# Kernel tuning notes

Hardware: AMD Instinct MI355X
Metric: run time of the kernel (lower is better)

Reference implementation:

```python
import jax, jax.numpy as jnp
import numpy as np

L, H, DH = 4, 8, 64            # num_layers, num_heads, hidden_dim (= dim_per_head)
HD = H * DH                    # 512 = per-layer q/k/v width
R, BLOCK, NREG, NW = 3, 128, 8, 8   # n_hashes, block_size, num_regions, num_w_per_dist
CDIM, LAT = 2, 3               # coords_dim, latent_dim
SCALE = 1.0 / float(np.sqrt(DH))


def layer_norm(x, g, b):
    m = x.mean(-1, keepdims=True)
    v = ((x - m) ** 2).mean(-1, keepdims=True)
    return (x - m) * jax.lax.rsqrt(v + 1e-5) * g + b


def hept_attention(q, k, v, coords, batch, w_head, hash_proj):
    # HEPT: E2LSH hash + region/batch bucketing -> sort -> blockwise attention
    # with RPE distance bias, combined over hash rounds by logsumexp weights.
    N = q.shape[0]
    nb = N // BLOCK
    qh = q.reshape(N, H, DH)
    kh = k.reshape(N, H, DH)
    vh = v.reshape(N, H, DH)
    c0 = coords[:, 0]
    region = jnp.clip(((c0 - c0.min()) / (c0.max() - c0.min() + 1e-6) * NREG).astype(jnp.int32), 0, NREG - 1)
    c_rpe = coords[:, 1:]                       # [N, CDIM-1] dims used for RPE distances
    bf = batch.astype(jnp.float32)
    outs, lses = [], []
    for r in range(R):
        hv = coords @ hash_proj[r]              # [N] LSH projection
        hn = (hv - hv.min()) / (hv.max() - hv.min() + 1e-6)
        skey = (bf * NREG + region.astype(jnp.float32)) * 2.0 + hn  # batch-major, region, hash
        idx = jnp.argsort(skey)
        inv = jnp.argsort(idx)
        qs = qh[idx].reshape(nb, BLOCK, H, DH)
        ks = kh[idx].reshape(nb, BLOCK, H, DH)
        vs = vh[idx].reshape(nb, BLOCK, H, DH)
        cs = c_rpe[idx].reshape(nb, BLOCK, CDIM - 1)
        bs = batch[idx].reshape(nb, BLOCK)
        scores = jnp.einsum('bihd,bjhd->bhij', qs, ks) * SCALE     # [nb,H,B,B]
        d2 = (cs[:, :, None, :] - cs[:, None, :, :]) ** 2          # [nb,B,B,CDIM-1]
        scores = scores - jnp.einsum('hc,bijc->bhij', w_head, d2)  # RPE distance penalty
        scores = jnp.where((bs[:, :, None] == bs[:, None, :])[:, None], scores, -1e9)
        lse = jax.nn.logsumexp(scores, axis=-1)                    # [nb,H,B]
        p = jnp.exp(scores - lse[..., None])
        o = jnp.einsum('bhij,bjhd->bihd', p, vs).reshape(N, H, DH)
        outs.append(o[inv])
        lses.append(jnp.transpose(lse, (0, 2, 1)).reshape(N, H)[inv])
    wts = jax.nn.softmax(jnp.stack(lses), axis=0)[..., None]       # [R,N,H,1]
    return (wts * jnp.stack(outs)).sum(0).reshape(N, HD)


def _forward(x, coords, batch, enc_W1, enc_b1, enc_W2, enc_b2, ln1_g, ln1_b, wq, wk, wv,
             rpe_W, wo, ln2_g, ln2_b, ff_W1, ff_b1, ff_W2, ff_b2, W_cat,
             mlp_W1, mlp_b1, mlp_W2, mlp_b2, beta_W1, beta_b1, beta_W2, beta_b2,
             coord_W1, coord_b1, coord_W2, coord_b2, hash_proj):
    h0 = jax.nn.relu(x @ enc_W1 + enc_b1) @ enc_W2 + enc_b2
    feats = [h0]
    cur = h0
    for l in range(L):
        xn = layer_norm(cur, ln1_g[l], ln1_b[l])
        q = xn @ wq[l]
        k = xn @ wk[l]
        v = xn @ wv[l]
        # per-head positive RPE weights derived from w_rpe weight matrix
        w_head = jax.nn.softplus(rpe_W[l].reshape(CDIM - 1, NW, H, DH).mean(axis=(1, 3)).T)  # [H,CDIM-1]
        a = hept_attention(q, k, v, coords, batch, w_head, hash_proj) @ wo[l]
        cur = cur + a
        ffo = jax.nn.relu(layer_norm(cur, ln2_g[l], ln2_b[l]) @ ff_W1[l] + ff_b1[l]) @ ff_W2[l] + ff_b2[l]
        cur = cur + ffo
        feats.append(cur)
    enc2 = jnp.concatenate(feats, axis=-1) @ W_cat
    out = enc2 + (jax.nn.relu(enc2 @ mlp_W1 + mlp_b1) @ mlp_W2 + mlp_b2)
    eps = 1e-6
    beta = jnp.clip(jax.nn.sigmoid(jax.nn.relu(out @ beta_W1 + beta_b1) @ beta_W2 + beta_b2), eps, 1.0 - eps)
    hcoord = jax.nn.relu(out @ coord_W1 + coord_b1) @ coord_W2 + coord_b2
    return beta, hcoord


def setup_inputs() -> dict:
    key = jax.random.key(0)
    ks = jax.random.split(key, 40)
    N, IN_DIM = 32768, 16
    def w(i, shape, s=0.05):
        return jax.random.normal(ks[i], shape, jnp.float32) * s
    return dict(
        x=jax.random.normal(ks[0], (N, IN_DIM), jnp.float32),
        coords=jax.random.normal(ks[1], (N, CDIM), jnp.float32),
        batch=jnp.sort(jax.random.randint(ks[2], (N,), 0, 8)),
        enc_W1=w(3, (IN_DIM, DH)), enc_b1=jnp.zeros((DH,), jnp.float32),
        enc_W2=w(4, (DH, DH)), enc_b2=jnp.zeros((DH,), jnp.float32),
        ln1_g=jnp.ones((L, DH), jnp.float32), ln1_b=jnp.zeros((L, DH), jnp.float32),
        wq=w(5, (L, DH, HD)), wk=w(6, (L, DH, HD)), wv=w(7, (L, DH, HD)),
        rpe_W=w(8, (L, NW * (CDIM - 1), HD)),
        wo=w(9, (L, HD, DH)),
        ln2_g=jnp.ones((L, DH), jnp.float32), ln2_b=jnp.zeros((L, DH), jnp.float32),
        ff_W1=w(10, (L, DH, DH)), ff_b1=jnp.zeros((L, DH), jnp.float32),
        ff_W2=w(11, (L, DH, DH)), ff_b2=jnp.zeros((L, DH), jnp.float32),
        W_cat=w(12, (DH * (L + 1), DH // 2)),
        mlp_W1=w(13, (DH // 2, DH // 2)), mlp_b1=jnp.zeros((DH // 2,), jnp.float32),
        mlp_W2=w(14, (DH // 2, DH // 2)), mlp_b2=jnp.zeros((DH // 2,), jnp.float32),
        beta_W1=w(15, (DH // 2, DH // 4)), beta_b1=jnp.zeros((DH // 4,), jnp.float32),
        beta_W2=w(16, (DH // 4, 1)), beta_b2=jnp.zeros((1,), jnp.float32),
        coord_W1=w(17, (DH // 2, DH // 4)), coord_b1=jnp.zeros((DH // 4,), jnp.float32),
        coord_W2=w(18, (DH // 4, LAT)), coord_b2=jnp.zeros((LAT,), jnp.float32),
        hash_proj=jax.random.normal(ks[19], (R, CDIM), jnp.float32),
    )


def reference(x, coords, batch, enc_W1, enc_b1, enc_W2, enc_b2, ln1_g, ln1_b, wq, wk, wv,
              rpe_W, wo, ln2_g, ln2_b, ff_W1, ff_b1, ff_W2, ff_b2, W_cat,
              mlp_W1, mlp_b1, mlp_W2, mlp_b2, beta_W1, beta_b1, beta_W2, beta_b2,
              coord_W1, coord_b1, coord_W2, coord_b2, hash_proj):
    return _forward(x, coords, batch, enc_W1, enc_b1, enc_W2, enc_b2, ln1_g, ln1_b, wq, wk, wv,
                    rpe_W, wo, ln2_g, ln2_b, ff_W1, ff_b1, ff_W2, ff_b2, W_cat,
                    mlp_W1, mlp_b1, mlp_W2, mlp_b2, beta_W1, beta_b1, beta_W2, beta_b2,
                    coord_W1, coord_b1, coord_W2, coord_b2, hash_proj)
```

## Files before the change

### kernel.cpp

```cpp
#include <hip/hip_runtime.h>
#include <math.h>

#define DEV __device__ __forceinline__

constexpr int DHc = 64;
constexpr int HDc = 512;
constexpr int Hc  = 8;
constexpr int BLKc = 128;

typedef float f32x16 __attribute__((ext_vector_type(16)));
typedef short s16x8  __attribute__((ext_vector_type(8)));

union FragU { unsigned u[4]; s16x8 v; };

DEV unsigned fenc(float f){ unsigned u = __float_as_uint(f); return (u & 0x80000000u) ? ~u : (u | 0x80000000u); }
DEV float fdec(unsigned u){ unsigned b = (u & 0x80000000u) ? (u ^ 0x80000000u) : ~u; return __uint_as_float(b); }
DEV float hv_calc(float c0, float c1, float h0, float h1){
  return __fadd_rn(__fmul_rn(c0, h0), __fmul_rn(c1, h1));
}
DEV unsigned short f2bf(float f){
  unsigned u = __float_as_uint(f);
  return (unsigned short)((u + 0x7FFFu + ((u >> 16) & 1u)) >> 16);
}
DEV float bf2f(unsigned short s){ return __uint_as_float((unsigned)s << 16); }

DEV unsigned cvtpk(float lo, float hi){
  unsigned r;
  asm("v_cvt_pk_bf16_f32 %0, %1, %2" : "=v"(r) : "v"(lo), "v"(hi));
  return r;
}
DEV void pswap(unsigned &a, unsigned &b){
  asm volatile("v_permlane32_swap_b32 %0, %1" : "+v"(a), "+v"(b));
}

__global__ void minmax_init_kernel(unsigned* mm){
  int t = threadIdx.x;
  if (t < 4) mm[t] = 0xFFFFFFFFu;
  else if (t < 8) mm[t] = 0u;
}

__global__ __launch_bounds__(256) void minmax_reduce_kernel(const float* __restrict__ coords,
    const float* __restrict__ hp, unsigned* mm, int N)
{
  __shared__ float red[4][8];
  float h[6];
  #pragma unroll
  for (int i = 0; i < 6; ++i) h[i] = hp[i];
  float mn[4] = {3.0e38f, 3.0e38f, 3.0e38f, 3.0e38f};
  float mx[4] = {-3.0e38f, -3.0e38f, -3.0e38f, -3.0e38f};
  for (int i = blockIdx.x*blockDim.x + threadIdx.x; i < N; i += gridDim.x*blockDim.x){
    float2 c = *(const float2*)&coords[2*i];
    float v0 = c.x;
    float v1 = hv_calc(c.x, c.y, h[0], h[1]);
    float v2 = hv_calc(c.x, c.y, h[2], h[3]);
    float v3 = hv_calc(c.x, c.y, h[4], h[5]);
    mn[0] = fminf(mn[0], v0); mx[0] = fmaxf(mx[0], v0);
    mn[1] = fminf(mn[1], v1); mx[1] = fmaxf(mx[1], v1);
    mn[2] = fminf(mn[2], v2); mx[2] = fmaxf(mx[2], v2);
    mn[3] = fminf(mn[3], v3); mx[3] = fmaxf(mx[3], v3);
  }
  #pragma unroll
  for (int o = 1; o < 64; o <<= 1){
    #pragma unroll
    for (int s = 0; s < 4; ++s){
      mn[s] = fminf(mn[s], __shfl_xor(mn[s], o));
      mx[s] = fmaxf(mx[s], __shfl_xor(mx[s], o));
    }
  }
  int w = threadIdx.x >> 6;
  if ((threadIdx.x & 63) == 0){
    #pragma unroll
    for (int s = 0; s < 4; ++s){ red[w][s] = mn[s]; red[w][4+s] = mx[s]; }
  }
  __syncthreads();
  int t = threadIdx.x;
  if (t < 4){
    float v = fminf(fminf(red[0][t], red[1][t]), fminf(red[2][t], red[3][t]));
    atomicMin(&mm[t], fenc(v));
  } else if (t < 8){
    float v = fmaxf(fmaxf(red[0][t], red[1][t]), fmaxf(red[2][t], red[3][t]));
    atomicMax(&mm[t], fenc(v));
  }
}

__global__ void make_keys_kernel(const float* __restrict__ coords, const int* __restrict__ batch,
                                 const float* __restrict__ hp, const unsigned* __restrict__ mm,
                                 unsigned long long* __restrict__ keys, int N)
{
  int i = blockIdx.x*blockDim.x + threadIdx.x;
  if (i >= N) return;
  float c0 = coords[2*i], c1 = coords[2*i+1];
  float c0min = fdec(mm[0]), c0max = fdec(mm[4]);
  float rf = (c0 - c0min) / (c0max - c0min + 1e-6f) * 8.0f;
  int region = (int)rf;
  region = region < 0 ? 0 : (region > 7 ? 7 : region);
  float base2 = ((float)batch[i] * 8.0f + (float)region) * 2.0f;
  #pragma unroll
  for (int r = 0; r < 3; ++r){
    float hv = hv_calc(c0, c1, hp[2*r], hp[2*r+1]);
    float hn = (hv - fdec(mm[1+r])) / (fdec(mm[5+r]) - fdec(mm[1+r]) + 1e-6f);
    float skey = base2 + hn;
    keys[(size_t)r*N + i] = ((unsigned long long)__float_as_uint(skey) << 32) | (unsigned)i;
  }
}

__global__ __launch_bounds__(1024) void bitonic_local_full2k_kernel(unsigned long long* keys, int N)
{
  __shared__ unsigned long long sh[2048];
  unsigned long long* a = keys + (size_t)blockIdx.y * N;
  int base = blockIdx.x * 2048, t = threadIdx.x;
  sh[t] = a[base + t];
  sh[t + 1024] = a[base + t + 1024];
  __syncthreads();
  for (int k = 2; k <= 2048; k <<= 1){
    for (int j = k >> 1; j > 0; j >>= 1){
      int i = ((t & ~(j-1)) << 1) | (t & (j-1));
      bool dirup = (((base + i) & k) == 0);
      unsigned long long x = sh[i], y = sh[i+j];
      if ((x > y) == dirup){ sh[i] = y; sh[i+j] = x; }
      __syncthreads();
    }
  }
  a[base + t] = sh[t];
  a[base + t + 1024] = sh[t + 1024];
}

__global__ void bitonic_global_kernel(unsigned long long* keys, int N, int k, int j)
{
  unsigned long long* a = keys + (size_t)blockIdx.y * N;
  int i = blockIdx.x*blockDim.x + threadIdx.x;
  int l = i ^ j;
  if (l > i && l < N){
    unsigned long long x = a[i], y = a[l];
    bool dirup = ((i & k) == 0);
    if ((x > y) == dirup){ a[i] = y; a[l] = x; }
  }
}

__global__ __launch_bounds__(1024) void bitonic_local_merge2k_kernel(unsigned long long* keys, int N, int k)
{
  __shared__ unsigned long long sh[2048];
  unsigned long long* a = keys + (size_t)blockIdx.y * N;
  int base = blockIdx.x * 2048, t = threadIdx.x;
  sh[t] = a[base + t];
  sh[t + 1024] = a[base + t + 1024];
  __syncthreads();
  for (int j = 1024; j > 0; j >>= 1){
    int i = ((t & ~(j-1)) << 1) | (t & (j-1));
    bool dirup = (((base + i) & k) == 0);
    unsigned long long x = sh[i], y = sh[i+j];
    if ((x > y) == dirup){ sh[i] = y; sh[i+j] = x; }
    __syncthreads();
  }
  a[base + t] = sh[t];
  a[base + t + 1024] = sh[t + 1024];
}

__global__ void extract_idx_kernel(const unsigned long long* __restrict__ keys, int* __restrict__ idx, int total)
{
  int i = blockIdx.x*blockDim.x + threadIdx.x;
  if (i < total) idx[i] = (int)(keys[i] & 0xFFFFFFFFull);
}

__global__ void wconv_kernel(const float* __restrict__ wq, const float* __restrict__ wk,
                             const float* __restrict__ wv, const float* __restrict__ wo,
                             unsigned short* __restrict__ wqkvT, unsigned short* __restrict__ woT)
{
  int tid = blockIdx.x*blockDim.x + threadIdx.x;
  const int NQ = 4*3*512*64;
  if (tid < NQ){
    int kk = tid & 63;
    int rest = tid >> 6;
    int n = rest & 511;
    int rest2 = rest >> 9;
    int z = rest2 % 3, l = rest2 / 3;
    const float* W = (z==0) ? wq : (z==1) ? wk : wv;
    wqkvT[tid] = f2bf(W[((size_t)l*64 + kk)*512 + n]);
  } else if (tid < NQ + 4*64*512){
    int e = tid - NQ;
    int kk = e & 511;
    int rest = e >> 9;
    int n = rest & 63;
    int l = rest >> 6;
    woT[e] = f2bf(wo[((size_t)l*512 + kk)*64 + n]);
  }
}

__global__ __launch_bounds__(256) void encoder_kernel(const float* __restrict__ x,
    const float* __restrict__ W1, const float* __restrict__ b1,
    const float* __restrict__ W2, const float* __restrict__ b2,
    const float* __restrict__ lng, const float* __restrict__ lnb,
    float* __restrict__ h0, unsigned short* __restrict__ xnb, int N)
{
  __shared__ float W1s[16][64];
  __shared__ __align__(16) float W2s[64][64];
  __shared__ float xs[4][16];
  __shared__ float t1s[4][64];
  int t = threadIdx.x;
  for (int f = t; f < 1024; f += 256) W1s[f>>6][f&63] = W1[f];
  #pragma unroll
  for (int e = 0; e < 4; ++e){ int f = t + e*256; *(float4*)&W2s[f>>4][(f&15)*4] = *(const float4*)&W2[f*4]; }
  int w = t >> 6, d = t & 63;
  int row = blockIdx.x*4 + w;
  if (d < 16) xs[w][d] = x[(size_t)row*16 + d];
  __syncthreads();
  float acc = b1[d];
  #pragma unroll
  for (int i = 0; i < 16; ++i) acc += xs[w][i]*W1s[i][d];
  t1s[w][d] = fmaxf(acc, 0.f);
  __syncthreads();
  float acc2 = b2[d];
  #pragma unroll
  for (int i = 0; i < 64; ++i) acc2 += t1s[w][i]*W2s[i][d];
  h0[(size_t)row*64 + d] = acc2;
  float s = acc2;
  #pragma unroll
  for (int o = 1; o < 64; o <<= 1) s += __shfl_xor(s, o);
  float mean = s * (1.0f/64.0f);
  float dv = acc2 - mean, sq = dv*dv;
  #pragma unroll
  for (int o = 1; o < 64; o <<= 1) sq += __shfl_xor(sq, o);
  xnb[(size_t)row*64 + d] = f2bf(dv * rsqrtf(sq*(1.0f/64.0f) + 1e-5f) * lng[d] + lnb[d]);
}

__global__ __launch_bounds__(256) void qkv_mfma_kernel(
    const unsigned short* __restrict__ xnb, const unsigned short* __restrict__ wqkvT_l,
    unsigned short* __restrict__ q, unsigned short* __restrict__ k, unsigned short* __restrict__ v, int N)
{
  __shared__ __align__(16) unsigned short a_lds[128*64];
  __shared__ __align__(16) unsigned short b_lds[128*64];
  int z = blockIdx.z;
  unsigned short* C = (z==0) ? q : (z==1) ? k : v;
  const unsigned short* wT = wqkvT_l + (size_t)z*512*64;
  float oscale = (z==0) ? 0.125f : 1.0f;
  int rb = blockIdx.x*128, cb = blockIdx.y*128;
  int t = threadIdx.x;
  #pragma unroll
  for (int e = 0; e < 4; ++e){
    int f = t + e*256; int row = f >> 3, ch = f & 7;
    *(s16x8*)&a_lds[row*64 + ((ch ^ (row&7))*8)] = *(const s16x8*)&xnb[(size_t)(rb+row)*64 + ch*8];
    *(s16x8*)&b_lds[row*64 + ((ch ^ (row&7))*8)] = *(const s16x8*)&wT[(size_t)(cb+row)*64 + ch*8];
  }
  __syncthreads();
  int w = t >> 6, l = t & 63, lo = l & 31, hi = l >> 5;
  s16x8 bf[4];
  #pragma unroll
  for (int ks = 0; ks < 4; ++ks){
    int brow = w*32 + lo, s = (ks<<1)|hi;
    bf[ks] = *(const s16x8*)&b_lds[brow*64 + ((s ^ (brow&7))*8)];
  }
  f32x16 acc[4];
  #pragma unroll
  for (int mt = 0; mt < 4; ++mt)
    #pragma unroll
    for (int i = 0; i < 16; ++i) acc[mt][i] = 0.f;
  #pragma unroll
  for (int mt = 0; mt < 4; ++mt){
    int arow = mt*32 + lo;
    #pragma unroll
    for (int ks = 0; ks < 4; ++ks){
      int s = (ks<<1)|hi;
      s16x8 af = *(const s16x8*)&a_lds[arow*64 + ((s ^ (arow&7))*8)];
      acc[mt] = __builtin_amdgcn_mfma_f32_32x32x16_bf16(af, bf[ks], acc[mt], 0, 0, 0);
    }
  }
  #pragma unroll
  for (int mt = 0; mt < 4; ++mt)
    #pragma unroll
    for (int reg = 0; reg < 16; ++reg){
      int m = mt*32 + (reg&3) + 8*(reg>>2) + 4*hi;
      C[(size_t)(rb+m)*HDc + cb + w*32 + lo] = f2bf(acc[mt][reg]*oscale);
    }
}

__global__ void whead_kernel(const float* __restrict__ rpe, float* __restrict__ wh)
{
  int l = blockIdx.x >> 3, h = blockIdx.x & 7, d = threadIdx.x;
  const float* rp = rpe + (size_t)l*8*512;
  float s = 0.f;
  #pragma unroll
  for (int w = 0; w < 8; ++w) s += rp[(size_t)w*512 + h*64 + d];
  #pragma unroll
  for (int o = 1; o < 64; o <<= 1) s += __shfl_xor(s, o);
  if (d == 0){
    float m = s * (1.0f/512.0f);
    wh[blockIdx.x] = fmaxf(m, 0.f) + log1pf(expf(-fabsf(m)));
  }
}

__global__ __launch_bounds__(256, 3) void attn_kernel(
    const unsigned short* __restrict__ qm, const unsigned short* __restrict__ km,
    const unsigned short* __restrict__ vm,
    const float* __restrict__ coords, const int* __restrict__ batch,
    const int* __restrict__ idx_all, const float* __restrict__ w_head,
    float* __restrict__ lse_all, unsigned short* __restrict__ o_buf, int N)
{
  __shared__ __align__(16) unsigned short qlds[128*64];
  __shared__ __align__(16) unsigned short klds[128*64];
  __shared__ __align__(16) unsigned short vtl[64*128];
  __shared__ __align__(16) float c1s[BLKc];
  __shared__ __align__(16) int   bts[BLKc];
  __shared__ int   idxs[BLKc];
  __shared__ __align__(16) float isel[BLKc];
  __shared__ int unif;
  int b = blockIdx.x, h = blockIdx.y, r = blockIdx.z, t = threadIdx.x;
  const int* idx_r = idx_all + (size_t)r*N;
  if (t < BLKc){
    int g = idx_r[b*BLKc + t];
    idxs[t] = g; c1s[t] = coords[2*g+1]; bts[t] = batch[g];
  }
  __syncthreads();
  if (t == 0) unif = (bts[0] == bts[127]);
  #pragma unroll
  for (int e = 0; e < 4; ++e){
    int f = t + e*256;
    int row = f >> 3, ch = f & 7;
    int g = idxs[row];
    s16x8 qv = *(const s16x8*)&qm[(size_t)g*HDc + h*DHc + ch*8];
    s16x8 kv = *(const s16x8*)&km[(size_t)g*HDc + h*DHc + ch*8];
    *(s16x8*)&qlds[row*64 + ((ch ^ (row&7))*8)] = qv;
    *(s16x8*)&klds[row*64 + ((ch ^ (row&7))*8)] = kv;
  }
  #pragma unroll
  for (int e = 0; e < 2; ++e){
    int pf = t + e*256;
    int jp = pf >> 3, dc = pf & 7;
    int j0 = jp*2, j1 = j0+1;
    s16x8 v0 = *(const s16x8*)&vm[(size_t)idxs[j0]*HDc + h*DHc + dc*8];
    s16x8 v1 = *(const s16x8*)&vm[(size_t)idxs[j1]*HDc + h*DHc + dc*8];
    int cj = jp >> 2;
    int jo = jp & 3;
    #pragma unroll
    for (int i = 0; i < 8; ++i){
      int d = dc*8 + i;
      unsigned val = (unsigned)(unsigned short)v0[i] | ((unsigned)(unsigned short)v1[i] << 16);
      *(unsigned*)&vtl[d*128 + ((cj ^ (d&7))*8) + jo*2] = val;
    }
  }
  __syncthreads();

  int w = t >> 6, l = t & 63, lo = l & 31, hi = l >> 5;
  int qrow = w*32 + lo;

  s16x8 qf[4];
  #pragma unroll
  for (int ks = 0; ks < 4; ++ks)
    qf[ks] = *(const s16x8*)&qlds[qrow*64 + ((((ks<<1)|hi) ^ (qrow&7))*8)];

  f32x16 acc[4];
  #pragma unroll
  for (int kt = 0; kt < 4; ++kt)
    #pragma unroll
    for (int i = 0; i < 16; ++i) acc[kt][i] = 0.f;

  __builtin_amdgcn_s_setprio(1);
  #pragma unroll
  for (int kt = 0; kt < 4; ++kt){
    int krow = kt*32 + lo;
    #pragma unroll
    for (int ks = 0; ks < 4; ++ks){
      s16x8 kf = *(const s16x8*)&klds[krow*64 + ((((ks<<1)|hi) ^ (krow&7))*8)];
      acc[kt] = __builtin_amdgcn_mfma_f32_32x32x16_bf16(kf, qf[ks], acc[kt], 0, 0, 0);
    }
  }
  __builtin_amdgcn_s_setprio(0);

  float c1i = c1s[qrow]; int bti = bts[qrow];
  float wh = w_head[h];
  int msk = unif;
  #pragma unroll
  for (int kt = 0; kt < 4; ++kt){
    #pragma unroll
    for (int rq = 0; rq < 4; ++rq){
      int kb = kt*32 + rq*8 + hi*4;
      float4 c4 = *(const float4*)&c1s[kb];
      int4  b4 = *(const int4*)&bts[kb];
      #pragma unroll
      for (int j = 0; j < 4; ++j){
        int reg = rq*4 + j;
        float c1k = (j==0)?c4.x:(j==1)?c4.y:(j==2)?c4.z:c4.w;
        int   btk = (j==0)?b4.x:(j==1)?b4.y:(j==2)?b4.z:b4.w;
        float dd = c1i - c1k;
        float sc = acc[kt][reg] - wh*dd*dd;
        if (!msk && bti != btk) sc = -1e9f;
        acc[kt][reg] = sc;
      }
    }
  }

  float m = -3.0e38f;
  #pragma unroll
  for (int kt = 0; kt < 4; ++kt)
    #pragma unroll
    for (int i = 0; i < 16; ++i) m = fmaxf(m, acc[kt][i]);
  m = fmaxf(m, __shfl_xor(m, 32));
  float se = 0.f;
  #pragma unroll
  for (int kt = 0; kt < 4; ++kt)
    #pragma unroll
    for (int i = 0; i < 16; ++i){
      float p = __expf(acc[kt][i] - m);
      acc[kt][i] = p;
      se += p;
    }
  se += __shfl_xor(se, 32);
  if (l < 32){
    int gi0 = idxs[qrow];
    lse_all[((size_t)r*N + gi0)*Hc + h] = m + __logf(se);
    isel[qrow] = 1.0f / se;
  }

  f32x16 oa0, oa1;
  #pragma unroll
  for (int i = 0; i < 16; ++i){ oa0[i] = 0.f; oa1[i] = 0.f; }

  __builtin_amdgcn_s_setprio(1);
  #pragma unroll
  for (int kt = 0; kt < 4; ++kt){
    unsigned X = cvtpk(acc[kt][0],  acc[kt][1]);
    unsigned Z = cvtpk(acc[kt][2],  acc[kt][3]);
    unsigned Y = cvtpk(acc[kt][4],  acc[kt][5]);
    unsigned W = cvtpk(acc[kt][6],  acc[kt][7]);
    pswap(X, Y); pswap(Z, W);
    FragU f0; f0.u[0]=X; f0.u[1]=Z; f0.u[2]=Y; f0.u[3]=W;
    unsigned X2 = cvtpk(acc[kt][8],  acc[kt][9]);
    unsigned Z2 = cvtpk(acc[kt][10], acc[kt][11]);
    unsigned Y2 = cvtpk(acc[kt][12], acc[kt][13]);
    unsigned W2 = cvtpk(acc[kt][14], acc[kt][15]);
    pswap(X2, Y2); pswap(Z2, W2);
    FragU f1; f1.u[0]=X2; f1.u[1]=Z2; f1.u[2]=Y2; f1.u[3]=W2;
    #pragma unroll
    for (int hks = 0; hks < 2; ++hks){
      s16x8 pa = hks ? f1.v : f0.v;
      int kch = kt*4 + hks*2 + hi;
      int d0 = lo;
      s16x8 vf0 = *(const s16x8*)&vtl[d0*128 + ((kch ^ (d0&7))*8)];
      oa0 = __builtin_amdgcn_mfma_f32_32x32x16_bf16(pa, vf0, oa0, 0, 0, 0);
      int d1 = 32 + lo;
      s16x8 vf1 = *(const s16x8*)&vtl[d1*128 + ((kch ^ (d1&7))*8)];
      oa1 = __builtin_amdgcn_mfma_f32_32x32x16_bf16(pa, vf1, oa1, 0, 0, 0);
    }
  }
  __builtin_amdgcn_s_setprio(0);

  unsigned short* orow = o_buf + (size_t)r*N*HDc;
  #pragma unroll
  for (int rq = 0; rq < 4; ++rq){
    float4 s4 = *(const float4*)&isel[w*32 + rq*8 + hi*4];
    #pragma unroll
    for (int j = 0; j < 4; ++j){
      int reg = rq*4 + j;
      int qq = rq*8 + hi*4 + j;
      int g = idxs[w*32 + qq];
      float sv = (j==0)?s4.x:(j==1)?s4.y:(j==2)?s4.z:s4.w;
      unsigned short* dst = &orow[(size_t)g*HDc + h*DHc + lo];
      dst[0]  = f2bf(oa0[reg]*sv);
      dst[32] = f2bf(oa1[reg]*sv);
    }
  }
}

__global__ __launch_bounds__(256) void wo_mfma_kernel(
    const unsigned short* __restrict__ o_buf, const float* __restrict__ lse_all,
    const unsigned short* __restrict__ woT_l, float* __restrict__ cur, int N)
{
  __shared__ __align__(16) unsigned short As[64*128];
  __shared__ __align__(16) unsigned short Bs[64*128];
  __shared__ float wts[64][24];
  int rb = blockIdx.x*64, t = threadIdx.x;
  #pragma unroll
  for (int e = 0; e < 2; ++e){
    int p = t + e*256;
    int rr = p >> 3, h = p & 7;
    float l0 = lse_all[((size_t)0*N + rb+rr)*Hc + h];
    float l1 = lse_all[((size_t)1*N + rb+rr)*Hc + h];
    float l2 = lse_all[((size_t)2*N + rb+rr)*Hc + h];
    float lm = fmaxf(l0, fmaxf(l1, l2));
    float e0 = __expf(l0-lm), e1 = __expf(l1-lm), e2 = __expf(l2-lm);
    float inv = 1.0f/(e0+e1+e2);
    wts[rr][h*3+0] = e0*inv; wts[rr][h*3+1] = e1*inv; wts[rr][h*3+2] = e2*inv;
  }
  int w = t >> 6, l = t & 63, lo = l & 31, hi = l >> 5;
  int mt = w >> 1, nt = w & 1;
  f32x16 acc;
  #pragma unroll
  for (int i = 0; i < 16; ++i) acc[i] = 0.f;
  for (int kt = 0; kt < 4; ++kt){
    __syncthreads();
    #pragma unroll
    for (int e = 0; e < 4; ++e){
      int f = t + e*256; int rr = f >> 4, kc = f & 15;
      int k0 = kt*128 + kc*8;
      int h = k0 >> 6;
      float w0 = wts[rr][h*3+0], w1 = wts[rr][h*3+1], w2 = wts[rr][h*3+2];
      s16x8 u0 = *(const s16x8*)&o_buf[((size_t)0*N + rb+rr)*HDc + k0];
      s16x8 u1 = *(const s16x8*)&o_buf[((size_t)1*N + rb+rr)*HDc + k0];
      s16x8 u2 = *(const s16x8*)&o_buf[((size_t)2*N + rb+rr)*HDc + k0];
      FragU fo;
      #pragma unroll
      for (int ii = 0; ii < 4; ++ii){
        float a0 = w0*bf2f((unsigned short)u0[2*ii])   + w1*bf2f((unsigned short)u1[2*ii])   + w2*bf2f((unsigned short)u2[2*ii]);
        float a1 = w0*bf2f((unsigned short)u0[2*ii+1]) + w1*bf2f((unsigned short)u1[2*ii+1]) + w2*bf2f((unsigned short)u2[2*ii+1]);
        fo.u[ii] = cvtpk(a0, a1);
      }
      *(s16x8*)&As[rr*128 + ((kc ^ (rr&7))*8)] = fo.v;
      *(s16x8*)&Bs[rr*128 + ((kc ^ (rr&7))*8)] = *(const s16x8*)&woT_l[(size_t)rr*512 + k0];
    }
    __syncthreads();
    #pragma unroll
    for (int ks = 0; ks < 8; ++ks){
      int s = ks*2 + hi;
      int arow = mt*32 + lo, brow = nt*32 + lo;
      s16x8 af = *(const s16x8*)&As[arow*128 + ((s ^ (arow&7))*8)];
      s16x8 bfr = *(const s16x8*)&Bs[brow*128 + ((s ^ (brow&7))*8)];
      acc = __builtin_amdgcn_mfma_f32_32x32x16_bf16(af, bfr, acc, 0, 0, 0);
    }
  }
  #pragma unroll
  for (int reg = 0; reg < 16; ++reg){
    int m = mt*32 + (reg&3) + 8*(reg>>2) + 4*hi;
    int n = nt*32 + lo;
    cur[(size_t)(rb+m)*64 + n] += acc[reg];
  }
}

__global__ __launch_bounds__(256) void ffn_kernel(float* __restrict__ cur,
    const float* __restrict__ g, const float* __restrict__ bln,
    const float* __restrict__ W1, const float* __restrict__ b1,
    const float* __restrict__ W2, const float* __restrict__ b2,
    const float* __restrict__ nlg, const float* __restrict__ nlb,
    unsigned short* __restrict__ xnb, int N)
{
  __shared__ __align__(16) float W1s[64][64];
  __shared__ __align__(16) float W2s[64][64];
  __shared__ float xns[4][64];
  __shared__ float t1s[4][64];
  int t = threadIdx.x;
  #pragma unroll
  for (int e = 0; e < 4; ++e){
    int f = t + e*256; int rr = f >> 4, c4 = f & 15;
    *(float4*)&W1s[rr][c4*4] = *(const float4*)&W1[f*4];
    *(float4*)&W2s[rr][c4*4] = *(const float4*)&W2[f*4];
  }
  int w = t >> 6, d = t & 63;
  int row = blockIdx.x*4 + w;
  float v = cur[(size_t)row*64 + d];
  float s = v;
  #pragma unroll
  for (int o = 1; o < 64; o <<= 1) s += __shfl_xor(s, o);
  float mean = s * (1.0f/64.0f);
  float dv = v - mean, sq = dv*dv;
  #pragma unroll
  for (int o = 1; o < 64; o <<= 1) sq += __shfl_xor(sq, o);
  float xnv = dv * rsqrtf(sq*(1.0f/64.0f) + 1e-5f) * g[d] + bln[d];
  xns[w][d] = xnv;
  __syncthreads();
  float acc = b1[d];
  #pragma unroll
  for (int i = 0; i < 64; ++i) acc += xns[w][i]*W1s[i][d];
  t1s[w][d] = fmaxf(acc, 0.f);
  __syncthreads();
  float acc2 = b2[d];
  #pragma unroll
  for (int i = 0; i < 64; ++i) acc2 += t1s[w][i]*W2s[i][d];
  float nv = v + acc2;
  cur[(size_t)row*64 + d] = nv;
  if (nlg){
    float s2 = nv;
    #pragma unroll
    for (int o = 1; o < 64; o <<= 1) s2 += __shfl_xor(s2, o);
    float mean2 = s2 * (1.0f/64.0f);
    float dv2 = nv - mean2, sq2 = dv2*dv2;
    #pragma unroll
    for (int o = 1; o < 64; o <<= 1) sq2 += __shfl_xor(sq2, o);
    xnb[(size_t)row*64 + d] = f2bf(dv2 * rsqrtf(sq2*(1.0f/64.0f) + 1e-5f) * nlg[d] + nlb[d]);
  }
}

__global__ __launch_bounds__(256) void enc2_accum_kernel(const float* __restrict__ cur,
    const float* __restrict__ Wcat, float* __restrict__ enc2, int rowoff, int store, int N)
{
  __shared__ float Ws[64][33];
  __shared__ float crs[32][65];
  int t = threadIdx.x;
  for (int f = t; f < 2048; f += 256) Ws[f>>5][f&31] = Wcat[(size_t)(rowoff + (f>>5))*32 + (f&31)];
  for (int f = t; f < 2048; f += 256) crs[f>>6][f&63] = cur[(size_t)(blockIdx.x*32 + (f>>6))*64 + (f&63)];
  __syncthreads();
  int r8 = t >> 5, c = t & 31;
  for (int rr = r8; rr < 32; rr += 8){
    int row = blockIdx.x*32 + rr;
    float acc = 0.f;
    #pragma unroll
    for (int d = 0; d < 64; ++d) acc += crs[rr][d]*Ws[d][c];
    size_t o = (size_t)row*32 + c;
    if (store) enc2[o] = acc; else enc2[o] += acc;
  }
}

__global__ __launch_bounds__(256) void head_kernel(const float* __restrict__ enc2,
    const float* mW1, const float* mb1, const float* mW2, const float* mb2,
    const float* bW1, const float* bb1, const float* bW2, const float* bb2,
    const float* cW1, const float* cb1, const float* cW2, const float* cb2,
    float* __restrict__ outp, int N)
{
  __shared__ float s_mW1[32][32], s_mW2[32][32], s_bW1[32][16], s_cW1[32][16];
  __shared__ float s_bW2[16], s_cW2[16][3];
  __shared__ float e2[8][32], t1[8][32], ov[8][32], bt[8][16], ct[8][16];
  int t = threadIdx.x;
  for (int f = t; f < 1024; f += 256){ s_mW1[f>>5][f&31] = mW1[f]; s_mW2[f>>5][f&31] = mW2[f]; }
  for (int f = t; f < 512; f += 256){ s_bW1[f>>4][f&15] = bW1[f]; s_cW1[f>>4][f&15] = cW1[f]; }
  if (t < 16) s_bW2[t] = bW2[t];
  if (t < 48) s_cW2[t/3][t%3] = cW2[t];
  int r8 = t >> 5, c = t & 31;
  int row = blockIdx.x*8 + r8;
  float e = enc2[(size_t)row*32 + c];
  e2[r8][c] = e;
  __syncthreads();
  float a = mb1[c];
  #pragma unroll
  for (int i = 0; i < 32; ++i) a += e2[r8][i]*s_mW1[i][c];
  t1[r8][c] = fmaxf(a, 0.f);
  __syncthreads();
  float o = e + mb2[c];
  #pragma unroll
  for (int i = 0; i < 32; ++i) o += t1[r8][i]*s_mW2[i][c];
  ov[r8][c] = o;
  __syncthreads();
  if (c < 16){
    float a2 = bb1[c];
    #pragma unroll
    for (int i = 0; i < 32; ++i) a2 += ov[r8][i]*s_bW1[i][c];
    bt[r8][c] = fmaxf(a2, 0.f);
  } else {
    int cc = c - 16;
    float a2 = cb1[cc];
    #pragma unroll
    for (int i = 0; i < 32; ++i) a2 += ov[r8][i]*s_cW1[i][cc];
    ct[r8][cc] = fmaxf(a2, 0.f);
  }
  __syncthreads();
  if (c == 0){
    float a3 = bb2[0];
    #pragma unroll
    for (int i = 0; i < 16; ++i) a3 += bt[r8][i]*s_bW2[i];
    float sg = 1.0f / (1.0f + __expf(-a3));
    sg = fminf(fmaxf(sg, 1e-6f), 1.0f - 1e-6f);
    outp[row] = sg;
  } else if (c < 4){
    int dd = c - 1;
    float a3 = cb2[dd];
    #pragma unroll
    for (int i = 0; i < 16; ++i) a3 += ct[r8][i]*s_cW2[i][dd];
    outp[(size_t)N + (size_t)row*3 + dd] = a3;
  }
}

extern "C" void kernel_launch(void* const* d_in, const int* in_sizes, int n_in,
                              void* d_out, int out_size, void* d_ws, size_t ws_size,
                              hipStream_t stream)
{
  const float* x       = (const float*)d_in[0];
  const float* coords  = (const float*)d_in[1];
  const int*   batch   = (const int*)d_in[2];
  const float* enc_W1  = (const float*)d_in[3];
  const float* enc_b1  = (const float*)d_in[4];
  const float* enc_W2  = (const float*)d_in[5];
  const float* enc_b2  = (const float*)d_in[6];
  const float* ln1_g   = (const float*)d_in[7];
  const float* ln1_b   = (const float*)d_in[8];
  const float* wq      = (const float*)d_in[9];
  const float* wk      = (const float*)d_in[10];
  const float* wv      = (const float*)d_in[11];
  const float* rpe_W   = (const float*)d_in[12];
  const float* wo      = (const float*)d_in[13];
  const float* ln2_g   = (const float*)d_in[14];
  const float* ln2_b   = (const float*)d_in[15];
  const float* ff_W1   = (const float*)d_in[16];
  const float* ff_b1   = (const float*)d_in[17];
  const float* ff_W2   = (const float*)d_in[18];
  const float* ff_b2   = (const float*)d_in[19];
  const float* W_cat   = (const float*)d_in[20];
  const float* mlp_W1  = (const float*)d_in[21];
  const float* mlp_b1  = (const float*)d_in[22];
  const float* mlp_W2  = (const float*)d_in[23];
  const float* mlp_b2  = (const float*)d_in[24];
  const float* beta_W1 = (const float*)d_in[25];
  const float* beta_b1 = (const float*)d_in[26];
  const float* beta_W2 = (const float*)d_in[27];
  const float* beta_b2 = (const float*)d_in[28];
  const float* coord_W1= (const float*)d_in[29];
  const float* coord_b1= (const float*)d_in[30];
  const float* coord_W2= (const float*)d_in[31];
  const float* coord_b2= (const float*)d_in[32];
  const float* hash_proj=(const float*)d_in[33];

  const int N  = in_sizes[0] / 16;
  const int nb = N / 128;
  float* outp = (float*)d_out;
  (void)out_size; (void)ws_size; (void)n_in;

  char* p = (char*)d_ws;
  size_t off = 0;
  auto alloc = [&](size_t bytes) -> char* {
    char* r = p + off;
    off += (bytes + 255) & ~(size_t)255;
    return r;
  };
  float* cur    = (float*)alloc((size_t)N*64*4);
  unsigned short* xnb = (unsigned short*)alloc((size_t)N*64*2);
  unsigned short* q = (unsigned short*)alloc((size_t)N*512*2);
  unsigned short* k = (unsigned short*)alloc((size_t)N*512*2);
  unsigned short* v = (unsigned short*)alloc((size_t)N*512*2);
  unsigned short* o_buf = (unsigned short*)alloc((size_t)3*N*512*2);
  float* enc2   = (float*)alloc((size_t)N*32*4);
  float* lse    = (float*)alloc((size_t)3*N*8*4);
  unsigned long long* keys = (unsigned long long*)alloc((size_t)3*N*8);
  int* idx      = (int*)alloc((size_t)3*N*4);
  unsigned short* wqkvT = (unsigned short*)alloc((size_t)4*3*512*64*2);
  unsigned short* woT   = (unsigned short*)alloc((size_t)4*64*512*2);
  unsigned* mm  = (unsigned*)alloc(256);
  float* whead  = (float*)alloc(256);

  wconv_kernel<<<2048, 256, 0, stream>>>(wq, wk, wv, wo, wqkvT, woT);
  whead_kernel<<<32, 64, 0, stream>>>(rpe_W, whead);

  minmax_init_kernel<<<1, 64, 0, stream>>>(mm);
  minmax_reduce_kernel<<<64, 256, 0, stream>>>(coords, hash_proj, mm, N);
  make_keys_kernel<<<(N+255)/256, 256, 0, stream>>>(coords, batch, hash_proj, mm, keys, N);
  bitonic_local_full2k_kernel<<<dim3(N/2048, 3), 1024, 0, stream>>>(keys, N);
  for (int kk = 4096; kk <= N; kk <<= 1){
    for (int j = kk >> 1; j >= 2048; j >>= 1)
      bitonic_global_kernel<<<dim3(N/256, 3), 256, 0, stream>>>(keys, N, kk, j);
    bitonic_local_merge2k_kernel<<<dim3(N/2048, 3), 1024, 0, stream>>>(keys, N, kk);
  }
  extract_idx_kernel<<<(3*N+255)/256, 256, 0, stream>>>(keys, idx, 3*N);

  encoder_kernel<<<N/4, 256, 0, stream>>>(x, enc_W1, enc_b1, enc_W2, enc_b2,
      ln1_g, ln1_b, cur, xnb, N);
  enc2_accum_kernel<<<N/32, 256, 0, stream>>>(cur, W_cat, enc2, 0, 1, N);

  for (int l = 0; l < 4; ++l){
    qkv_mfma_kernel<<<dim3(N/128, 4, 3), 256, 0, stream>>>(xnb,
        wqkvT + (size_t)l*3*512*64, q, k, v, N);
    attn_kernel<<<dim3(nb, 8, 3), 256, 0, stream>>>(q, k, v, coords, batch,
        idx, whead + l*8, lse, o_buf, N);
    wo_mfma_kernel<<<N/64, 256, 0, stream>>>(o_buf, lse, woT + (size_t)l*64*512, cur, N);
    const float* nlg = (l < 3) ? (ln1_g + (l+1)*64) : nullptr;
    const float* nlb = (l < 3) ? (ln1_b + (l+1)*64) : nullptr;
    ffn_kernel<<<N/4, 256, 0, stream>>>(cur, ln2_g + l*64, ln2_b + l*64,
        ff_W1 + (size_t)l*64*64, ff_b1 + l*64, ff_W2 + (size_t)l*64*64, ff_b2 + l*64,
        nlg, nlb, xnb, N);
    enc2_accum_kernel<<<N/32, 256, 0, stream>>>(cur, W_cat, enc2, (l+1)*64, 0, N);
  }

  head_kernel<<<N/8, 256, 0, stream>>>(enc2, mlp_W1, mlp_b1, mlp_W2, mlp_b2,
      beta_W1, beta_b1, beta_W2, beta_b2, coord_W1, coord_b1, coord_W2, coord_b2, outp, N);
}
```

Measured before the change: 800.4 us.

## Fuse QKV projection into attention kernel, computing per-head Q/K/V from gathered inputs

Drops the separate QKV GEMM kernel and the global q/k/v buffers. Each attention block gathers its 128 sorted rows of the normalized input (64-wide) and computes Q, K and V for its head with MFMA directly into LDS, writing V transposed. The 1/sqrt(d) scale is folded into the converted Q weights. This removes a large write and gather of N×512 bf16 tensors per layer. In exchange the projection is recomputed three times, once per hash round, and the weights are read from global memory per block.

```diff
diff --git a/kernel.cpp b/kernel.cpp
--- a/kernel.cpp
+++ b/kernel.cpp
@@ -28,6 +28,9 @@
   unsigned r;
   asm("v_cvt_pk_bf16_f32 %0, %1, %2" : "=v"(r) : "v"(lo), "v"(hi));
   return r;
+}
+DEV unsigned pack_bf2(float lo, float hi){
+  return (unsigned)f2bf(lo) | ((unsigned)f2bf(hi) << 16);
 }
 DEV void pswap(unsigned &a, unsigned &b){
   asm volatile("v_permlane32_swap_b32 %0, %1" : "+v"(a), "+v"(b));
@@ -175,7 +178,8 @@
     int rest2 = rest >> 9;
     int z = rest2 % 3, l = rest2 / 3;
     const float* W = (z==0) ? wq : (z==1) ? wk : wv;
-    wqkvT[tid] = f2bf(W[((size_t)l*64 + kk)*512 + n]);
+    float scale = (z==0) ? 0.125f : 1.0f;
+    wqkvT[tid] = f2bf(W[((size_t)l*64 + kk)*512 + n] * scale);
   } else if (tid < NQ + 4*64*512){
     int e = tid - NQ;
     int kk = e & 511;
@@ -223,56 +227,6 @@
   xnb[(size_t)row*64 + d] = f2bf(dv * rsqrtf(sq*(1.0f/64.0f) + 1e-5f) * lng[d] + lnb[d]);
 }
 
-__global__ __launch_bounds__(256) void qkv_mfma_kernel(
-    const unsigned short* __restrict__ xnb, const unsigned short* __restrict__ wqkvT_l,
-    unsigned short* __restrict__ q, unsigned short* __restrict__ k, unsigned short* __restrict__ v, int N)
-{
-  __shared__ __align__(16) unsigned short a_lds[128*64];
-  __shared__ __align__(16) unsigned short b_lds[128*64];
-  int z = blockIdx.z;
-  unsigned short* C = (z==0) ? q : (z==1) ? k : v;
-  const unsigned short* wT = wqkvT_l + (size_t)z*512*64;
-  float oscale = (z==0) ? 0.125f : 1.0f;
-  int rb = blockIdx.x*128, cb = blockIdx.y*128;
-  int t = threadIdx.x;
-  #pragma unroll
-  for (int e = 0; e < 4; ++e){
-    int f = t + e*256; int row = f >> 3, ch = f & 7;
-    *(s16x8*)&a_lds[row*64 + ((ch ^ (row&7))*8)] = *(const s16x8*)&xnb[(size_t)(rb+row)*64 + ch*8];
-    *(s16x8*)&b_lds[row*64 + ((ch ^ (row&7))*8)] = *(const s16x8*)&wT[(size_t)(cb+row)*64 + ch*8];
-  }
-  __syncthreads();
-  int w = t >> 6, l = t & 63, lo = l & 31, hi = l >> 5;
-  s16x8 bf[4];
-  #pragma unroll
-  for (int ks = 0; ks < 4; ++ks){
-    int brow = w*32 + lo, s = (ks<<1)|hi;
-    bf[ks] = *(const s16x8*)&b_lds[brow*64 + ((s ^ (brow&7))*8)];
-  }
-  f32x16 acc[4];
-  #pragma unroll
-  for (int mt = 0; mt < 4; ++mt)
-    #pragma unroll
-    for (int i = 0; i < 16; ++i) acc[mt][i] = 0.f;
-  #pragma unroll
-  for (int mt = 0; mt < 4; ++mt){
-    int arow = mt*32 + lo;
-    #pragma unroll
-    for (int ks = 0; ks < 4; ++ks){
-      int s = (ks<<1)|hi;
-      s16x8 af = *(const s16x8*)&a_lds[arow*64 + ((s ^ (arow&7))*8)];
-      acc[mt] = __builtin_amdgcn_mfma_f32_32x32x16_bf16(af, bf[ks], acc[mt], 0, 0, 0);
-    }
-  }
-  #pragma unroll
-  for (int mt = 0; mt < 4; ++mt)
-    #pragma unroll
-    for (int reg = 0; reg < 16; ++reg){
-      int m = mt*32 + (reg&3) + 8*(reg>>2) + 4*hi;
-      C[(size_t)(rb+m)*HDc + cb + w*32 + lo] = f2bf(acc[mt][reg]*oscale);
-    }
-}
-
 __global__ void whead_kernel(const float* __restrict__ rpe, float* __restrict__ wh)
 {
   int l = blockIdx.x >> 3, h = blockIdx.x & 7, d = threadIdx.x;
@@ -289,8 +243,7 @@
 }
 
 __global__ __launch_bounds__(256, 3) void attn_kernel(
-    const unsigned short* __restrict__ qm, const unsigned short* __restrict__ km,
-    const unsigned short* __restrict__ vm,
+    const unsigned short* __restrict__ xnb, const unsigned short* __restrict__ wqkvT_l,
     const float* __restrict__ coords, const int* __restrict__ batch,
     const int* __restrict__ idx_all, const float* __restrict__ w_head,
     float* __restrict__ lse_all, unsigned short* __restrict__ o_buf, int N)
@@ -311,37 +264,57 @@
   }
   __syncthreads();
   if (t == 0) unif = (bts[0] == bts[127]);
-  #pragma unroll
-  for (int e = 0; e < 4; ++e){
-    int f = t + e*256;
-    int row = f >> 3, ch = f & 7;
-    int g = idxs[row];
-    s16x8 qv = *(const s16x8*)&qm[(size_t)g*HDc + h*DHc + ch*8];
-    s16x8 kv = *(const s16x8*)&km[(size_t)g*HDc + h*DHc + ch*8];
-    *(s16x8*)&qlds[row*64 + ((ch ^ (row&7))*8)] = qv;
-    *(s16x8*)&klds[row*64 + ((ch ^ (row&7))*8)] = kv;
-  }
-  #pragma unroll
-  for (int e = 0; e < 2; ++e){
-    int pf = t + e*256;
-    int jp = pf >> 3, dc = pf & 7;
-    int j0 = jp*2, j1 = j0+1;
-    s16x8 v0 = *(const s16x8*)&vm[(size_t)idxs[j0]*HDc + h*DHc + dc*8];
-    s16x8 v1 = *(const s16x8*)&vm[(size_t)idxs[j1]*HDc + h*DHc + dc*8];
-    int cj = jp >> 2;
-    int jo = jp & 3;
-    #pragma unroll
-    for (int i = 0; i < 8; ++i){
-      int d = dc*8 + i;
-      unsigned val = (unsigned)(unsigned short)v0[i] | ((unsigned)(unsigned short)v1[i] << 16);
-      *(unsigned*)&vtl[d*128 + ((cj ^ (d&7))*8) + jo*2] = val;
-    }
-  }
-  __syncthreads();
 
   int w = t >> 6, l = t & 63, lo = l & 31, hi = l >> 5;
+
+  int gm = idxs[w*32 + lo];
+  const unsigned short* arp = &xnb[(size_t)gm*64];
+  s16x8 af[4];
+  #pragma unroll
+  for (int ks = 0; ks < 4; ++ks)
+    af[ks] = *(const s16x8*)&arp[ks*16 + hi*8];
+
+  const unsigned short* whb = wqkvT_l + (size_t)h*64*64;
+  #pragma unroll
+  for (int z = 0; z < 3; ++z){
+    const unsigned short* wz = whb + (size_t)z*512*64;
+    f32x16 a0, a1;
+    #pragma unroll
+    for (int i = 0; i < 16; ++i){ a0[i] = 0.f; a1[i] = 0.f; }
+    #pragma unroll
+    for (int ks = 0; ks < 4; ++ks){
+      s16x8 b0 = *(const s16x8*)&wz[(size_t)(lo)*64      + ks*16 + hi*8];
+      s16x8 b1 = *(const s16x8*)&wz[(size_t)(32 + lo)*64 + ks*16 + hi*8];
+      a0 = __builtin_amdgcn_mfma_f32_32x32x16_bf16(af[ks], b0, a0, 0, 0, 0);
+      a1 = __builtin_amdgcn_mfma_f32_32x32x16_bf16(af[ks], b1, a1, 0, 0, 0);
+    }
+    if (z < 2){
+      unsigned short* dst = z ? klds : qlds;
+      int ch0 = lo >> 3, ch1 = 4 + (lo >> 3), co = lo & 7;
+      #pragma unroll
+      for (int reg = 0; reg < 16; ++reg){
+        int row = w*32 + (reg&3) + 8*(reg>>2) + 4*hi;
+        dst[row*64 + ((ch0 ^ (row&7))*8) + co] = f2bf(a0[reg]);
+        dst[row*64 + ((ch1 ^ (row&7))*8) + co] = f2bf(a1[reg]);
+      }
+    } else {
+      #pragma unroll
+      for (int rq = 0; rq < 4; ++rq){
+        int k0 = w*32 + rq*8 + 4*hi;
+        int cj = k0 >> 3;
+        int d0 = lo, d1 = 32 + lo;
+        unsigned* dp0 = (unsigned*)&vtl[d0*128 + ((cj ^ (d0&7))*8) + 4*hi];
+        dp0[0] = pack_bf2(a0[rq*4+0], a0[rq*4+1]);
+        dp0[1] = pack_bf2(a0[rq*4+2], a0[rq*4+3]);
+        unsigned* dp1 = (unsigned*)&vtl[d1*128 + ((cj ^ (d1&7))*8) + 4*hi];
+        dp1[0] = pack_bf2(a1[rq*4+0], a1[rq*4+1]);
+        dp1[1] = pack_bf2(a1[rq*4+2], a1[rq*4+3]);
+      }
+    }
+  }
+  __syncthreads();
+
   int qrow = w*32 + lo;
-
   s16x8 qf[4];
   #pragma unroll
   for (int ks = 0; ks < 4; ++ks)
@@ -458,6 +431,7 @@
       dst[32] = f2bf(oa1[reg]*sv);
     }
   }
+  (void)b;
 }
 
 __global__ __launch_bounds__(256) void wo_mfma_kernel(
@@ -708,9 +682,6 @@
   };
   float* cur    = (float*)alloc((size_t)N*64*4);
   unsigned short* xnb = (unsigned short*)alloc((size_t)N*64*2);
-  unsigned short* q = (unsigned short*)alloc((size_t)N*512*2);
-  unsigned short* k = (unsigned short*)alloc((size_t)N*512*2);
-  unsigned short* v = (unsigned short*)alloc((size_t)N*512*2);
   unsigned short* o_buf = (unsigned short*)alloc((size_t)3*N*512*2);
   float* enc2   = (float*)alloc((size_t)N*32*4);
   float* lse    = (float*)alloc((size_t)3*N*8*4);
@@ -740,10 +711,8 @@
   enc2_accum_kernel<<<N/32, 256, 0, stream>>>(cur, W_cat, enc2, 0, 1, N);
 
   for (int l = 0; l < 4; ++l){
-    qkv_mfma_kernel<<<dim3(N/128, 4, 3), 256, 0, stream>>>(xnb,
-        wqkvT + (size_t)l*3*512*64, q, k, v, N);
-    attn_kernel<<<dim3(nb, 8, 3), 256, 0, stream>>>(q, k, v, coords, batch,
-        idx, whead + l*8, lse, o_buf, N);
+    attn_kernel<<<dim3(nb, 8, 3), 256, 0, stream>>>(xnb,
+        wqkvT + (size_t)l*3*512*64, coords, batch, idx, whead + l*8, lse, o_buf, N);
     wo_mfma_kernel<<<N/64, 256, 0, stream>>>(o_buf, lse, woT + (size_t)l*64*512, cur, N);
     const float* nlg = (l < 3) ? (ln1_g + (l+1)*64) : nullptr;
     const float* nlb = (l < 3) ? (ln1_b + (l+1)*64) : nullptr;
```

Result: no change. 787.7 us (-1.6%).
